# Optimization experiments

Hardware: AMD Instinct MI355X
Metric: run time of the kernel (lower is better)

Reference implementation:

```python
import jax, jax.numpy as jnp
import numpy as np

EPS = 1e-5

def _mvn(feat):
    # instance-norm style mean/std over spatial dims; torch .var is unbiased (ddof=1)
    b, c = feat.shape[:2]
    flat = feat.reshape(b, c, -1)
    mu = flat.mean(-1)[:, :, None, None]
    std = jnp.sqrt(flat.var(-1, ddof=1) + EPS)[:, :, None, None]
    return (feat - mu) / std

def setup_inputs() -> dict:
    key = jax.random.key(0)
    ks = jax.random.split(key, 10)
    B, C, H, W = 4, 512, 64, 64
    sc = 0.05
    return {
        "content": jax.random.normal(ks[0], (B, C, H, W), jnp.float32),
        "style": jax.random.normal(ks[1], (B, C, H, W), jnp.float32),
        "content_key": jax.random.normal(ks[2], (B, C, H, W), jnp.float32),
        "style_key": jax.random.normal(ks[3], (B, C, H, W), jnp.float32),
        "Wf": jax.random.normal(ks[4], (C, C), jnp.float32) * sc,
        "bf": jax.random.normal(ks[5], (C,), jnp.float32) * sc,
        "Wg": jax.random.normal(ks[6], (C, C), jnp.float32) * sc,
        "bg": jax.random.normal(ks[7], (C,), jnp.float32) * sc,
        "Wh": jax.random.normal(ks[8], (C, C), jnp.float32) * sc,
        "bh": jax.random.normal(ks[9], (C,), jnp.float32) * sc,
    }

def reference(content, style, content_key, style_key, Wf, bf, Wg, bg, Wh, bh):
    b, C, h, w = content.shape
    hs, ws = style.shape[2], style.shape[3]
    n, m = h * w, hs * ws
    # 1x1 convs are per-pixel linear maps
    Fq = jnp.einsum('oc,bcn->bno', Wf, content_key.reshape(b, -1, n)) + bf      # [b, n, ck]
    G = jnp.einsum('oc,bcn->bon', Wg, style_key.reshape(b, -1, m)) + bg[:, None]  # [b, ck, m]
    V = jnp.einsum('oc,bcn->bno', Wh, style.reshape(b, C, m)) + bh              # [b, m, C]
    S = jax.nn.softmax(jnp.einsum('bnc,bcm->bnm', Fq, G), axis=-1)              # [b, n, m]
    mean = jnp.einsum('bnm,bmc->bnc', S, V)                                     # attention-weighted mean
    m2 = jnp.einsum('bnm,bmc->bnc', S, V * V)                                   # weighted second moment
    std = jnp.sqrt(jax.nn.relu(m2 - mean * mean))
    mean = mean.reshape(b, h, w, C).transpose(0, 3, 1, 2)
    std = std.reshape(b, h, w, C).transpose(0, 3, 1, 2)
    return std * _mvn(content) + mean
```

## Files before the change

kernel.cpp:

```cpp
#include <hip/hip_runtime.h>
#include <math.h>

#define BATCH 4
#define C 512
#define N 4096
#define M 4096
#define MSPLIT 4

typedef __attribute__((ext_vector_type(8))) short short8;
typedef __attribute__((ext_vector_type(8))) __bf16 bf16x8;
typedef __attribute__((ext_vector_type(4))) float f32x4;

static __device__ __forceinline__ unsigned short f2bf(float x) {
    unsigned u = __float_as_uint(x);
    u += 0x7fff + ((u >> 16) & 1);
    return (unsigned short)(u >> 16);
}
static __device__ __forceinline__ float bf2f(unsigned short h) {
    return __uint_as_float(((unsigned)h) << 16);
}
static __device__ __forceinline__ f32x4 mfma_bf16(short8 a, short8 b, f32x4 c) {
    return __builtin_amdgcn_mfma_f32_16x16x32_bf16(
        __builtin_bit_cast(bf16x8, a), __builtin_bit_cast(bf16x8, b), c, 0, 0, 0);
}

__global__ __launch_bounds__(256) void wsplit_kernel(
    const float* __restrict__ W, unsigned short* __restrict__ hi,
    unsigned short* __restrict__ lo)
{
    int i = blockIdx.x * 256 + threadIdx.x;
    float v = W[i];
    unsigned short h = f2bf(v);
    hi[i] = h;
    lo[i] = f2bf(v - bf2f(h));
}

__global__ __launch_bounds__(256) void linear_fg_mfma(
    const float* __restrict__ in,
    const unsigned short* __restrict__ Whi, const unsigned short* __restrict__ Wlo,
    const float* __restrict__ bias,
    unsigned short* __restrict__ out_hi, unsigned short* __restrict__ out_lo)
{
    __shared__ float in_s[32][68];
    __shared__ __align__(16) unsigned short wh_s[64][40];
    __shared__ __align__(16) unsigned short wl_s[64][40];
    const int tid = threadIdx.x;
    const int n0 = blockIdx.x * 64, o0 = blockIdx.y * 64;
    const int w = tid >> 6, lane = tid & 63;
    const int wrow = w >> 1, wcol = w & 1;
    const int lr = lane & 15, q = lane >> 4;
    f32x4 acc[2][2];
    #pragma unroll
    for (int i = 0; i < 2; ++i)
        #pragma unroll
        for (int j = 0; j < 2; ++j) acc[i][j] = (f32x4){0.f, 0.f, 0.f, 0.f};

    for (int kc = 0; kc < C; kc += 32) {
        __syncthreads();
        #pragma unroll
        for (int it = 0; it < 2; ++it) {
            int idx = tid + it * 256;
            int k = idx >> 4, seg = idx & 15;
            *(float4*)&in_s[k][seg * 4] =
                *(const float4*)&in[(size_t)(kc + k) * N + n0 + seg * 4];
        }
        {
            int o = tid >> 2, sg = tid & 3;
            *(float4*)&wh_s[o][sg * 8] = *(const float4*)&Whi[(size_t)(o0 + o) * 512 + kc + sg * 8];
            *(float4*)&wl_s[o][sg * 8] = *(const float4*)&Wlo[(size_t)(o0 + o) * 512 + kc + sg * 8];
        }
        __syncthreads();
        short8 ah[2], al[2], bh[2], bl[2];
        #pragma unroll
        for (int i = 0; i < 2; ++i) {
            int n = wrow * 32 + i * 16 + lr;
            #pragma unroll
            for (int j = 0; j < 8; ++j) {
                float f = in_s[q * 8 + j][n];
                unsigned short h = f2bf(f);
                ah[i][j] = (short)h;
                al[i][j] = (short)f2bf(f - bf2f(h));
            }
        }
        #pragma unroll
        for (int j = 0; j < 2; ++j) {
            int o = wcol * 32 + j * 16 + lr;
            bh[j] = *(const short8*)&wh_s[o][q * 8];
            bl[j] = *(const short8*)&wl_s[o][q * 8];
        }
        #pragma unroll
        for (int i = 0; i < 2; ++i)
            #pragma unroll
            for (int j = 0; j < 2; ++j) {
                acc[i][j] = mfma_bf16(ah[i], bh[j], acc[i][j]);
                acc[i][j] = mfma_bf16(ah[i], bl[j], acc[i][j]);
                acc[i][j] = mfma_bf16(al[i], bh[j], acc[i][j]);
            }
    }
    #pragma unroll
    for (int i = 0; i < 2; ++i)
        #pragma unroll
        for (int j = 0; j < 2; ++j) {
            int o = o0 + wcol * 32 + j * 16 + lr;
            float bo = bias[o];
            #pragma unroll
            for (int r = 0; r < 4; ++r) {
                int n = n0 + wrow * 32 + i * 16 + q * 4 + r;
                float v = acc[i][j][r] + bo;
                unsigned short h = f2bf(v);
                out_hi[(size_t)n * 512 + o] = h;
                out_lo[(size_t)n * 512 + o] = f2bf(v - bf2f(h));
            }
        }
}

__global__ __launch_bounds__(256) void linear_v_mfma(
    const float* __restrict__ in,
    const unsigned short* __restrict__ Whi, const unsigned short* __restrict__ Wlo,
    const float* __restrict__ bias,
    unsigned short* __restrict__ vhT, unsigned short* __restrict__ v2hT,
    unsigned short* __restrict__ v2lT)
{
    __shared__ float in_s[32][68];
    __shared__ __align__(16) unsigned short wh_s[64][40];
    __shared__ __align__(16) unsigned short wl_s[64][40];
    const int tid = threadIdx.x;
    const int m0 = blockIdx.x * 64, o0 = blockIdx.y * 64;
    const int w = tid >> 6, lane = tid & 63;
    const int wrow = w >> 1, wcol = w & 1;
    const int lr = lane & 15, q = lane >> 4;
    f32x4 acc[2][2];
    #pragma unroll
    for (int i = 0; i < 2; ++i)
        #pragma unroll
        for (int j = 0; j < 2; ++j) acc[i][j] = (f32x4){0.f, 0.f, 0.f, 0.f};

    for (int kc = 0; kc < C; kc += 32) {
        __syncthreads();
        #pragma unroll
        for (int it = 0; it < 2; ++it) {
            int idx = tid + it * 256;
            int k = idx >> 4, seg = idx & 15;
            *(float4*)&in_s[k][seg * 4] =
                *(const float4*)&in[(size_t)(kc + k) * N + m0 + seg * 4];
        }
        {
            int o = tid >> 2, sg = tid & 3;
            *(float4*)&wh_s[o][sg * 8] = *(const float4*)&Whi[(size_t)(o0 + o) * 512 + kc + sg * 8];
            *(float4*)&wl_s[o][sg * 8] = *(const float4*)&Wlo[(size_t)(o0 + o) * 512 + kc + sg * 8];
        }
        __syncthreads();
        short8 ah[2], al[2], bh[2], bl[2];
        #pragma unroll
        for (int i = 0; i < 2; ++i) {
            int o = wrow * 32 + i * 16 + lr;
            ah[i] = *(const short8*)&wh_s[o][q * 8];
            al[i] = *(const short8*)&wl_s[o][q * 8];
        }
        #pragma unroll
        for (int j = 0; j < 2; ++j) {
            int m = wcol * 32 + j * 16 + lr;
            #pragma unroll
            for (int t = 0; t < 8; ++t) {
                float f = in_s[q * 8 + t][m];
                unsigned short h = f2bf(f);
                bh[j][t] = (short)h;
                bl[j][t] = (short)f2bf(f - bf2f(h));
            }
        }
        #pragma unroll
        for (int i = 0; i < 2; ++i)
            #pragma unroll
            for (int j = 0; j < 2; ++j) {
                acc[i][j] = mfma_bf16(ah[i], bh[j], acc[i][j]);
                acc[i][j] = mfma_bf16(ah[i], bl[j], acc[i][j]);
                acc[i][j] = mfma_bf16(al[i], bh[j], acc[i][j]);
            }
    }
    #pragma unroll
    for (int i = 0; i < 2; ++i)
        #pragma unroll
        for (int r = 0; r < 4; ++r) {
            int o = o0 + wrow * 32 + i * 16 + q * 4 + r;
            float bo = bias[o];
            #pragma unroll
            for (int j = 0; j < 2; ++j) {
                int m = m0 + wcol * 32 + j * 16 + lr;
                float v = acc[i][j][r] + bo;
                unsigned short vh = f2bf(v);
                float vhf = bf2f(vh);
                float vsq = vhf * vhf;
                unsigned short v2h = f2bf(vsq);
                unsigned short v2l = f2bf(vsq - bf2f(v2h));
                size_t off = (size_t)o * M + m;
                vhT[off] = vh;
                v2hT[off] = v2h;
                v2lT[off] = v2l;
            }
        }
}

__global__ __launch_bounds__(256) void logits_mfma_kernel(
    const unsigned short* __restrict__ Ah, const unsigned short* __restrict__ Al,
    const unsigned short* __restrict__ Bh, const unsigned short* __restrict__ Bl,
    float* __restrict__ S)
{
    __shared__ __align__(16) unsigned short Ah_s[128 * 40];
    __shared__ __align__(16) unsigned short Al_s[128 * 40];
    __shared__ __align__(16) unsigned short Bh_s[128 * 40];
    __shared__ __align__(16) unsigned short Bl_s[128 * 40];
    const int tid = threadIdx.x;
    const int n0 = blockIdx.y * 128, m0 = blockIdx.x * 128;
    const int w = tid >> 6, lane = tid & 63;
    const int wrow = w >> 1, wcol = w & 1;
    const int lr = lane & 15, q = lane >> 4;
    f32x4 acc[4][4];
    #pragma unroll
    for (int i = 0; i < 4; ++i)
        #pragma unroll
        for (int j = 0; j < 4; ++j)
            acc[i][j] = (f32x4){0.f, 0.f, 0.f, 0.f};

    for (int kc = 0; kc < C; kc += 32) {
        __syncthreads();
        #pragma unroll
        for (int it = 0; it < 2; ++it) {
            int idx = tid + it * 256;
            int row = idx >> 2, seg = idx & 3;
            int ldso = row * 40 + seg * 8;
            int go = kc + seg * 8;
            *(float4*)&Ah_s[ldso] = *(const float4*)&Ah[(size_t)(n0 + row) * C + go];
            *(float4*)&Al_s[ldso] = *(const float4*)&Al[(size_t)(n0 + row) * C + go];
            *(float4*)&Bh_s[ldso] = *(const float4*)&Bh[(size_t)(m0 + row) * C + go];
            *(float4*)&Bl_s[ldso] = *(const float4*)&Bl[(size_t)(m0 + row) * C + go];
        }
        __syncthreads();
        short8 ah[4], al[4], bh[4], bl[4];
        #pragma unroll
        for (int i = 0; i < 4; ++i) {
            int ro = (wrow * 64 + i * 16 + lr) * 40 + q * 8;
            int co = (wcol * 64 + i * 16 + lr) * 40 + q * 8;
            ah[i] = *(const short8*)&Ah_s[ro];
            al[i] = *(const short8*)&Al_s[ro];
            bh[i] = *(const short8*)&Bh_s[co];
            bl[i] = *(const short8*)&Bl_s[co];
        }
        #pragma unroll
        for (int i = 0; i < 4; ++i)
            #pragma unroll
            for (int j = 0; j < 4; ++j) {
                acc[i][j] = mfma_bf16(ah[i], bh[j], acc[i][j]);
                acc[i][j] = mfma_bf16(ah[i], bl[j], acc[i][j]);
                acc[i][j] = mfma_bf16(al[i], bh[j], acc[i][j]);
            }
    }
    #pragma unroll
    for (int i = 0; i < 4; ++i) {
        int nb = n0 + wrow * 64 + i * 16 + q * 4;
        #pragma unroll
        for (int j = 0; j < 4; ++j) {
            int m = m0 + wcol * 64 + j * 16 + lr;
            #pragma unroll
            for (int r = 0; r < 4; ++r)
                S[(size_t)(nb + r) * M + m] = acc[i][j][r];
        }
    }
}

__global__ __launch_bounds__(256) void rowstat_p_kernel(
    const float* __restrict__ S, unsigned short* __restrict__ P,
    float* __restrict__ rsum)
{
    const int n = blockIdx.x;
    const int tid = threadIdx.x;
    const float* row = S + (size_t)n * M;
    float v[16];
    #pragma unroll
    for (int i = 0; i < 16; ++i) v[i] = row[tid + i * 256];
    float lm = -INFINITY;
    #pragma unroll
    for (int i = 0; i < 16; ++i) lm = fmaxf(lm, v[i]);
    #pragma unroll
    for (int off = 32; off > 0; off >>= 1) lm = fmaxf(lm, __shfl_xor(lm, off, 64));
    __shared__ float red[4];
    __shared__ float redsum[4];
    const int wid = tid >> 6, lane = tid & 63;
    if (lane == 0) red[wid] = lm;
    __syncthreads();
    const float rm = fmaxf(fmaxf(red[0], red[1]), fmaxf(red[2], red[3]));
    float ls = 0.f;
    unsigned short* prow = P + (size_t)n * M;
    #pragma unroll
    for (int i = 0; i < 16; ++i) {
        float p = __expf(v[i] - rm);
        unsigned short pb = f2bf(p);
        prow[tid + i * 256] = pb;
        ls += bf2f(pb);
    }
    #pragma unroll
    for (int off = 32; off > 0; off >>= 1) ls += __shfl_xor(ls, off, 64);
    if (lane == 0) redsum[wid] = ls;
    __syncthreads();
    if (tid == 0) rsum[n] = redsum[0] + redsum[1] + redsum[2] + redsum[3];
}

__global__ __launch_bounds__(256) void apply_partial_kernel(
    const unsigned short* __restrict__ P, const unsigned short* __restrict__ VhT,
    const unsigned short* __restrict__ V2hT, const unsigned short* __restrict__ V2lT,
    float* __restrict__ accm_p, float* __restrict__ acc2_p)
{
    __shared__ __align__(16) unsigned short P_s[128 * 40];
    __shared__ __align__(16) unsigned short Vh_s[64 * 40];
    __shared__ __align__(16) unsigned short V2h_s[64 * 40];
    __shared__ __align__(16) unsigned short V2l_s[64 * 40];
    const int tid = threadIdx.x;
    const int c0 = blockIdx.x * 64, n0 = blockIdx.y * 128;
    const int z = blockIdx.z;
    const int w = tid >> 6, lane = tid & 63;
    const int wrow = w >> 1, wcol = w & 1;
    const int lr = lane & 15, q = lane >> 4;
    f32x4 accm[4][2], acc2[4][2];
    #pragma unroll
    for (int i = 0; i < 4; ++i)
        #pragma unroll
        for (int j = 0; j < 2; ++j) {
            accm[i][j] = (f32x4){0.f, 0.f, 0.f, 0.f};
            acc2[i][j] = (f32x4){0.f, 0.f, 0.f, 0.f};
        }

    const int mbeg = z * (M / MSPLIT);
    for (int mc = mbeg; mc < mbeg + M / MSPLIT; mc += 32) {
        __syncthreads();
        #pragma unroll
        for (int it = 0; it < 2; ++it) {
            int idx = tid + it * 256;
            int row = idx >> 2, seg = idx & 3;
            *(float4*)&P_s[row * 40 + seg * 8] =
                *(const float4*)&P[(size_t)(n0 + row) * M + mc + seg * 8];
        }
        {
            int row = tid >> 2, seg = tid & 3;
            int ldso = row * 40 + seg * 8;
            size_t go = (size_t)(c0 + row) * M + mc + seg * 8;
            *(float4*)&Vh_s[ldso]  = *(const float4*)&VhT[go];
            *(float4*)&V2h_s[ldso] = *(const float4*)&V2hT[go];
            *(float4*)&V2l_s[ldso] = *(const float4*)&V2lT[go];
        }
        __syncthreads();
        short8 a[4], bmat[2], b2h[2], b2l[2];
        #pragma unroll
        for (int i = 0; i < 4; ++i)
            a[i] = *(const short8*)&P_s[(wrow * 64 + i * 16 + lr) * 40 + q * 8];
        #pragma unroll
        for (int j = 0; j < 2; ++j) {
            int co = (wcol * 32 + j * 16 + lr) * 40 + q * 8;
            bmat[j] = *(const short8*)&Vh_s[co];
            b2h[j]  = *(const short8*)&V2h_s[co];
            b2l[j]  = *(const short8*)&V2l_s[co];
        }
        #pragma unroll
        for (int i = 0; i < 4; ++i)
            #pragma unroll
            for (int j = 0; j < 2; ++j) {
                accm[i][j] = mfma_bf16(a[i], bmat[j], accm[i][j]);
                acc2[i][j] = mfma_bf16(a[i], b2h[j],  acc2[i][j]);
                acc2[i][j] = mfma_bf16(a[i], b2l[j],  acc2[i][j]);
            }
    }
    const size_t pbase = (size_t)z * N * C;
    #pragma unroll
    for (int i = 0; i < 4; ++i) {
        int nb = n0 + wrow * 64 + i * 16 + q * 4;
        #pragma unroll
        for (int j = 0; j < 2; ++j) {
            int c = c0 + wcol * 32 + j * 16 + lr;
            #pragma unroll
            for (int r = 0; r < 4; ++r) {
                size_t off = pbase + (size_t)(nb + r) * C + c;
                accm_p[off] = accm[i][j][r];
                acc2_p[off] = acc2[i][j][r];
            }
        }
    }
}

__global__ __launch_bounds__(256) void combine_kernel(
    const float* __restrict__ accm_p, const float* __restrict__ acc2_p,
    const float* __restrict__ rsum, float* __restrict__ meanw,
    float* __restrict__ stdw)
{
    const size_t idx = ((size_t)blockIdx.x * 256 + threadIdx.x) * 4;
    const int n = (int)(idx >> 9);
    const float inv = 1.0f / rsum[n];
    float sm[4] = {0.f, 0.f, 0.f, 0.f}, s2[4] = {0.f, 0.f, 0.f, 0.f};
    #pragma unroll
    for (int z = 0; z < MSPLIT; ++z) {
        float4 a = *(const float4*)&accm_p[(size_t)z * N * C + idx];
        float4 b = *(const float4*)&acc2_p[(size_t)z * N * C + idx];
        sm[0] += a.x; sm[1] += a.y; sm[2] += a.z; sm[3] += a.w;
        s2[0] += b.x; s2[1] += b.y; s2[2] += b.z; s2[3] += b.w;
    }
    float4 mnv, sdv;
    float* mp = (float*)&mnv;
    float* sp = (float*)&sdv;
    #pragma unroll
    for (int k = 0; k < 4; ++k) {
        float mn = sm[k] * inv;
        float m2 = s2[k] * inv;
        mp[k] = mn;
        sp[k] = sqrtf(fmaxf(m2 - mn * mn, 0.f));
    }
    *(float4*)&meanw[idx] = mnv;
    *(float4*)&stdw[idx]  = sdv;
}

__global__ __launch_bounds__(256) void mvn_kernel(
    const float* __restrict__ content, float* __restrict__ mu, float* __restrict__ rstd)
{
    const int c = blockIdx.x;
    const int tid = threadIdx.x;
    const float* row = content + (size_t)c * N;
    float s = 0.f, ss = 0.f;
    for (int i = tid; i < N; i += 256) {
        float v = row[i];
        s += v;
        ss = fmaf(v, v, ss);
    }
    #pragma unroll
    for (int off = 32; off > 0; off >>= 1) {
        s  += __shfl_xor(s,  off, 64);
        ss += __shfl_xor(ss, off, 64);
    }
    __shared__ float rs[4], rss[4];
    const int wid = tid >> 6, lane = tid & 63;
    if (lane == 0) { rs[wid] = s; rss[wid] = ss; }
    __syncthreads();
    if (tid == 0) {
        float st = rs[0] + rs[1] + rs[2] + rs[3];
        float sst = rss[0] + rss[1] + rss[2] + rss[3];
        float m = st / (float)N;
        float var = (sst - st * st / (float)N) / (float)(N - 1);
        mu[c] = m;
        rstd[c] = rsqrtf(var + 1e-5f);
    }
}

__global__ __launch_bounds__(256) void final_kernel(
    const float* __restrict__ content, const float* __restrict__ meanw,
    const float* __restrict__ stdw, const float* __restrict__ mu,
    const float* __restrict__ rstd, float* __restrict__ out)
{
    __shared__ float mn_s[32][33], sd_s[32][33];
    const int tid = threadIdx.x;
    const int n0 = blockIdx.x * 32;
    const int c0 = blockIdx.y * 32;
    const int tx = tid & 31, ty = tid >> 5;
    #pragma unroll
    for (int i = 0; i < 4; ++i) {
        int n = ty + i * 8;
        mn_s[tx][n] = meanw[(size_t)(n0 + n) * C + c0 + tx];
        sd_s[tx][n] = stdw [(size_t)(n0 + n) * C + c0 + tx];
    }
    __syncthreads();
    #pragma unroll
    for (int i = 0; i < 4; ++i) {
        int c = ty + i * 8;
        float m = mu[c0 + c], r = rstd[c0 + c];
        size_t off = (size_t)(c0 + c) * N + n0 + tx;
        float x = content[off];
        out[off] = sd_s[c][tx] * (x - m) * r + mn_s[c][tx];
    }
}

extern "C" void kernel_launch(void* const* d_in, const int* in_sizes, int n_in,
                              void* d_out, int out_size, void* d_ws, size_t ws_size,
                              hipStream_t stream)
{
    const float* content = (const float*)d_in[0];
    const float* style   = (const float*)d_in[1];
    const float* ckey    = (const float*)d_in[2];
    const float* skey    = (const float*)d_in[3];
    const float* Wf      = (const float*)d_in[4];
    const float* bf      = (const float*)d_in[5];
    const float* Wg      = (const float*)d_in[6];
    const float* bg      = (const float*)d_in[7];
    const float* Wh      = (const float*)d_in[8];
    const float* bh      = (const float*)d_in[9];
    float* out = (float*)d_out;

    const size_t sz_w  = (size_t)512 * 512 * 2;
    const size_t sz_S  = (size_t)N * M * 4;
    const size_t sz_FG = (size_t)N * C * 2;
    const size_t sz_P  = (size_t)N * M * 2;
    const size_t sz_V  = (size_t)C * M * 2;

    char* p = (char*)d_ws;
    auto alloc = [&](size_t bytes) {
        char* r = p;
        p += (bytes + 255) & ~(size_t)255;
        return r;
    };
    unsigned short* WfH = (unsigned short*)alloc(sz_w);
    unsigned short* WfL = (unsigned short*)alloc(sz_w);
    unsigned short* WgH = (unsigned short*)alloc(sz_w);
    unsigned short* WgL = (unsigned short*)alloc(sz_w);
    unsigned short* WhH = (unsigned short*)alloc(sz_w);
    unsigned short* WhL = (unsigned short*)alloc(sz_w);
    float* S = (float*)alloc(sz_S);
    unsigned short* Fh = (unsigned short*)alloc(sz_FG);
    unsigned short* Fl = (unsigned short*)alloc(sz_FG);
    unsigned short* Gh = (unsigned short*)alloc(sz_FG);
    unsigned short* Gl = (unsigned short*)alloc(sz_FG);
    unsigned short* P    = (unsigned short*)alloc(sz_P);
    unsigned short* VhT  = (unsigned short*)alloc(sz_V);
    unsigned short* V2hT = (unsigned short*)alloc(sz_V);
    unsigned short* V2lT = (unsigned short*)alloc(sz_V);
    float* rsum  = (float*)alloc((size_t)N * 4);
    float* meanw = (float*)alloc((size_t)N * C * 4);
    float* stdw  = (float*)alloc((size_t)N * C * 4);
    float* mu    = (float*)alloc((size_t)C * 4);
    float* rstd  = (float*)alloc((size_t)C * 4);

    float* accm_p = S;
    float* acc2_p = S + (size_t)MSPLIT * N * C;

    wsplit_kernel<<<dim3(1024), 256, 0, stream>>>(Wf, WfH, WfL);
    wsplit_kernel<<<dim3(1024), 256, 0, stream>>>(Wg, WgH, WgL);
    wsplit_kernel<<<dim3(1024), 256, 0, stream>>>(Wh, WhH, WhL);

    for (int b = 0; b < BATCH; ++b) {
        const size_t fo = (size_t)b * C * N;
        linear_fg_mfma<<<dim3(N / 64, C / 64), 256, 0, stream>>>(ckey + fo, WfH, WfL, bf, Fh, Fl);
        linear_fg_mfma<<<dim3(M / 64, C / 64), 256, 0, stream>>>(skey + fo, WgH, WgL, bg, Gh, Gl);
        linear_v_mfma<<<dim3(M / 64, C / 64), 256, 0, stream>>>(style + fo, WhH, WhL, bh,
                                                                VhT, V2hT, V2lT);
        logits_mfma_kernel<<<dim3(M / 128, N / 128), 256, 0, stream>>>(Fh, Fl, Gh, Gl, S);
        rowstat_p_kernel<<<dim3(N), 256, 0, stream>>>(S, P, rsum);
        apply_partial_kernel<<<dim3(C / 64, N / 128, MSPLIT), 256, 0, stream>>>(
            P, VhT, V2hT, V2lT, accm_p, acc2_p);
        combine_kernel<<<dim3(N * C / 1024), 256, 0, stream>>>(
            accm_p, acc2_p, rsum, meanw, stdw);
        mvn_kernel<<<dim3(C), 256, 0, stream>>>(content + fo, mu, rstd);
        final_kernel<<<dim3(N / 32, C / 32), 256, 0, stream>>>(
            content + fo, meanw, stdw, mu, rstd, out + fo);
    }
}
```

Before: 1.145 ms.

## Use direct global-to-LDS loads and compute V squared splits on the fly

The logits and apply kernels now stage tiles through global_load_lds (16-byte direct-to-LDS loads) in an unpadded 32-wide LDS layout instead of loading through registers into padded rows. The V-projection kernel no longer writes the V² hi/lo bf16 arrays. The apply kernel rebuilds V² hi/lo from the bf16 V tile in registers with packed bf16 conversions, which cuts global traffic and LDS usage. The cost is extra ALU work per tile and possible LDS bank conflicts from dropping the padding.

```diff
diff --git a/kernel.cpp b/kernel.cpp
--- a/kernel.cpp
+++ b/kernel.cpp
@@ -10,6 +10,7 @@
 typedef __attribute__((ext_vector_type(8))) short short8;
 typedef __attribute__((ext_vector_type(8))) __bf16 bf16x8;
 typedef __attribute__((ext_vector_type(4))) float f32x4;
+typedef __attribute__((ext_vector_type(4))) unsigned int uint4v;
 
 static __device__ __forceinline__ unsigned short f2bf(float x) {
     unsigned u = __float_as_uint(x);
@@ -22,6 +23,16 @@
 static __device__ __forceinline__ f32x4 mfma_bf16(short8 a, short8 b, f32x4 c) {
     return __builtin_amdgcn_mfma_f32_16x16x32_bf16(
         __builtin_bit_cast(bf16x8, a), __builtin_bit_cast(bf16x8, b), c, 0, 0, 0);
+}
+static __device__ __forceinline__ void gload16(const void* g, void* l) {
+    __builtin_amdgcn_global_load_lds(
+        (const __attribute__((address_space(1))) void*)g,
+        (__attribute__((address_space(3))) void*)l, 16, 0, 0);
+}
+static __device__ __forceinline__ unsigned cvt_pk_bf16(float a, float b) {
+    unsigned r;
+    asm("v_cvt_pk_bf16_f32 %0, %1, %2" : "=v"(r) : "v"(a), "v"(b));
+    return r;
 }
 
 __global__ __launch_bounds__(256) void wsplit_kernel(
@@ -118,8 +129,7 @@
     const float* __restrict__ in,
     const unsigned short* __restrict__ Whi, const unsigned short* __restrict__ Wlo,
     const float* __restrict__ bias,
-    unsigned short* __restrict__ vhT, unsigned short* __restrict__ v2hT,
-    unsigned short* __restrict__ v2lT)
+    unsigned short* __restrict__ vhT)
 {
     __shared__ float in_s[32][68];
     __shared__ __align__(16) unsigned short wh_s[64][40];
@@ -187,15 +197,7 @@
             for (int j = 0; j < 2; ++j) {
                 int m = m0 + wcol * 32 + j * 16 + lr;
                 float v = acc[i][j][r] + bo;
-                unsigned short vh = f2bf(v);
-                float vhf = bf2f(vh);
-                float vsq = vhf * vhf;
-                unsigned short v2h = f2bf(vsq);
-                unsigned short v2l = f2bf(vsq - bf2f(v2h));
-                size_t off = (size_t)o * M + m;
-                vhT[off] = vh;
-                v2hT[off] = v2h;
-                v2lT[off] = v2l;
+                vhT[(size_t)o * M + m] = f2bf(v);
             }
         }
 }
@@ -205,15 +207,16 @@
     const unsigned short* __restrict__ Bh, const unsigned short* __restrict__ Bl,
     float* __restrict__ S)
 {
-    __shared__ __align__(16) unsigned short Ah_s[128 * 40];
-    __shared__ __align__(16) unsigned short Al_s[128 * 40];
-    __shared__ __align__(16) unsigned short Bh_s[128 * 40];
-    __shared__ __align__(16) unsigned short Bl_s[128 * 40];
+    __shared__ __align__(16) unsigned short Ah_s[128 * 32];
+    __shared__ __align__(16) unsigned short Al_s[128 * 32];
+    __shared__ __align__(16) unsigned short Bh_s[128 * 32];
+    __shared__ __align__(16) unsigned short Bl_s[128 * 32];
     const int tid = threadIdx.x;
     const int n0 = blockIdx.y * 128, m0 = blockIdx.x * 128;
     const int w = tid >> 6, lane = tid & 63;
     const int wrow = w >> 1, wcol = w & 1;
     const int lr = lane & 15, q = lane >> 4;
+    const int srow = lane >> 2, scol = (lane & 3) * 8;
     f32x4 acc[4][4];
     #pragma unroll
     for (int i = 0; i < 4; ++i)
@@ -224,22 +227,22 @@
     for (int kc = 0; kc < C; kc += 32) {
         __syncthreads();
         #pragma unroll
-        for (int it = 0; it < 2; ++it) {
-            int idx = tid + it * 256;
-            int row = idx >> 2, seg = idx & 3;
-            int ldso = row * 40 + seg * 8;
-            int go = kc + seg * 8;
-            *(float4*)&Ah_s[ldso] = *(const float4*)&Ah[(size_t)(n0 + row) * C + go];
-            *(float4*)&Al_s[ldso] = *(const float4*)&Al[(size_t)(n0 + row) * C + go];
-            *(float4*)&Bh_s[ldso] = *(const float4*)&Bh[(size_t)(m0 + row) * C + go];
-            *(float4*)&Bl_s[ldso] = *(const float4*)&Bl[(size_t)(m0 + row) * C + go];
+        for (int g2 = 0; g2 < 2; ++g2) {
+            int g = w * 2 + g2;
+            size_t ga = (size_t)(n0 + g * 16 + srow) * C + kc + scol;
+            size_t gb = (size_t)(m0 + g * 16 + srow) * C + kc + scol;
+            int lo = g * 512;
+            gload16(&Ah[ga], &Ah_s[lo]);
+            gload16(&Al[ga], &Al_s[lo]);
+            gload16(&Bh[gb], &Bh_s[lo]);
+            gload16(&Bl[gb], &Bl_s[lo]);
         }
         __syncthreads();
         short8 ah[4], al[4], bh[4], bl[4];
         #pragma unroll
         for (int i = 0; i < 4; ++i) {
-            int ro = (wrow * 64 + i * 16 + lr) * 40 + q * 8;
-            int co = (wcol * 64 + i * 16 + lr) * 40 + q * 8;
+            int ro = (wrow * 64 + i * 16 + lr) * 32 + q * 8;
+            int co = (wcol * 64 + i * 16 + lr) * 32 + q * 8;
             ah[i] = *(const short8*)&Ah_s[ro];
             al[i] = *(const short8*)&Al_s[ro];
             bh[i] = *(const short8*)&Bh_s[co];
@@ -306,19 +309,17 @@
 
 __global__ __launch_bounds__(256) void apply_partial_kernel(
     const unsigned short* __restrict__ P, const unsigned short* __restrict__ VhT,
-    const unsigned short* __restrict__ V2hT, const unsigned short* __restrict__ V2lT,
     float* __restrict__ accm_p, float* __restrict__ acc2_p)
 {
-    __shared__ __align__(16) unsigned short P_s[128 * 40];
-    __shared__ __align__(16) unsigned short Vh_s[64 * 40];
-    __shared__ __align__(16) unsigned short V2h_s[64 * 40];
-    __shared__ __align__(16) unsigned short V2l_s[64 * 40];
+    __shared__ __align__(16) unsigned short P_s[128 * 32];
+    __shared__ __align__(16) unsigned short Vh_s[64 * 32];
     const int tid = threadIdx.x;
     const int c0 = blockIdx.x * 64, n0 = blockIdx.y * 128;
     const int z = blockIdx.z;
     const int w = tid >> 6, lane = tid & 63;
     const int wrow = w >> 1, wcol = w & 1;
     const int lr = lane & 15, q = lane >> 4;
+    const int srow = lane >> 2, scol = (lane & 3) * 8;
     f32x4 accm[4][2], acc2[4][2];
     #pragma unroll
     for (int i = 0; i < 4; ++i)
@@ -332,39 +333,42 @@
     for (int mc = mbeg; mc < mbeg + M / MSPLIT; mc += 32) {
         __syncthreads();
         #pragma unroll
-        for (int it = 0; it < 2; ++it) {
-            int idx = tid + it * 256;
-            int row = idx >> 2, seg = idx & 3;
-            *(float4*)&P_s[row * 40 + seg * 8] =
-                *(const float4*)&P[(size_t)(n0 + row) * M + mc + seg * 8];
-        }
-        {
-            int row = tid >> 2, seg = tid & 3;
-            int ldso = row * 40 + seg * 8;
-            size_t go = (size_t)(c0 + row) * M + mc + seg * 8;
-            *(float4*)&Vh_s[ldso]  = *(const float4*)&VhT[go];
-            *(float4*)&V2h_s[ldso] = *(const float4*)&V2hT[go];
-            *(float4*)&V2l_s[ldso] = *(const float4*)&V2lT[go];
-        }
-        __syncthreads();
-        short8 a[4], bmat[2], b2h[2], b2l[2];
+        for (int g2 = 0; g2 < 2; ++g2) {
+            int g = w * 2 + g2;
+            gload16(&P[(size_t)(n0 + g * 16 + srow) * M + mc + scol], &P_s[g * 512]);
+        }
+        gload16(&VhT[(size_t)(c0 + w * 16 + srow) * M + mc + scol], &Vh_s[w * 512]);
+        __syncthreads();
+        short8 a[4], bh[2], b2h[2], b2l[2];
         #pragma unroll
         for (int i = 0; i < 4; ++i)
-            a[i] = *(const short8*)&P_s[(wrow * 64 + i * 16 + lr) * 40 + q * 8];
+            a[i] = *(const short8*)&P_s[(wrow * 64 + i * 16 + lr) * 32 + q * 8];
         #pragma unroll
         for (int j = 0; j < 2; ++j) {
-            int co = (wcol * 32 + j * 16 + lr) * 40 + q * 8;
-            bmat[j] = *(const short8*)&Vh_s[co];
-            b2h[j]  = *(const short8*)&V2h_s[co];
-            b2l[j]  = *(const short8*)&V2l_s[co];
+            bh[j] = *(const short8*)&Vh_s[(wcol * 32 + j * 16 + lr) * 32 + q * 8];
+            uint4v u = __builtin_bit_cast(uint4v, bh[j]);
+            uint4v hv, lv;
+            #pragma unroll
+            for (int t = 0; t < 4; ++t) {
+                float v0 = __uint_as_float(u[t] << 16);
+                float v1 = __uint_as_float(u[t] & 0xffff0000u);
+                float s0 = v0 * v0, s1 = v1 * v1;
+                unsigned hh = cvt_pk_bf16(s0, s1);
+                float r0 = s0 - __uint_as_float(hh << 16);
+                float r1 = s1 - __uint_as_float(hh & 0xffff0000u);
+                hv[t] = hh;
+                lv[t] = cvt_pk_bf16(r0, r1);
+            }
+            b2h[j] = __builtin_bit_cast(short8, hv);
+            b2l[j] = __builtin_bit_cast(short8, lv);
         }
         #pragma unroll
         for (int i = 0; i < 4; ++i)
             #pragma unroll
             for (int j = 0; j < 2; ++j) {
-                accm[i][j] = mfma_bf16(a[i], bmat[j], accm[i][j]);
-                acc2[i][j] = mfma_bf16(a[i], b2h[j],  acc2[i][j]);
-                acc2[i][j] = mfma_bf16(a[i], b2l[j],  acc2[i][j]);
+                accm[i][j] = mfma_bf16(a[i], bh[j],  accm[i][j]);
+                acc2[i][j] = mfma_bf16(a[i], b2h[j], acc2[i][j]);
+                acc2[i][j] = mfma_bf16(a[i], b2l[j], acc2[i][j]);
             }
     }
     const size_t pbase = (size_t)z * N * C;
@@ -513,8 +517,6 @@
     unsigned short* Gl = (unsigned short*)alloc(sz_FG);
     unsigned short* P    = (unsigned short*)alloc(sz_P);
     unsigned short* VhT  = (unsigned short*)alloc(sz_V);
-    unsigned short* V2hT = (unsigned short*)alloc(sz_V);
-    unsigned short* V2lT = (unsigned short*)alloc(sz_V);
     float* rsum  = (float*)alloc((size_t)N * 4);
     float* meanw = (float*)alloc((size_t)N * C * 4);
     float* stdw  = (float*)alloc((size_t)N * C * 4);
@@ -532,12 +534,11 @@
         const size_t fo = (size_t)b * C * N;
         linear_fg_mfma<<<dim3(N / 64, C / 64), 256, 0, stream>>>(ckey + fo, WfH, WfL, bf, Fh, Fl);
         linear_fg_mfma<<<dim3(M / 64, C / 64), 256, 0, stream>>>(skey + fo, WgH, WgL, bg, Gh, Gl);
-        linear_v_mfma<<<dim3(M / 64, C / 64), 256, 0, stream>>>(style + fo, WhH, WhL, bh,
-                                                                VhT, V2hT, V2lT);
+        linear_v_mfma<<<dim3(M / 64, C / 64), 256, 0, stream>>>(style + fo, WhH, WhL, bh, VhT);
         logits_mfma_kernel<<<dim3(M / 128, N / 128), 256, 0, stream>>>(Fh, Fl, Gh, Gl, S);
         rowstat_p_kernel<<<dim3(N), 256, 0, stream>>>(S, P, rsum);
         apply_partial_kernel<<<dim3(C / 64, N / 128, MSPLIT), 256, 0, stream>>>(
-            P, VhT, V2hT, V2lT, accm_p, acc2_p);
+            P, VhT, accm_p, acc2_p);
         combine_kernel<<<dim3(N * C / 1024), 256, 0, stream>>>(
             accm_p, acc2_p, rsum, meanw, stdw);
         mvn_kernel<<<dim3(C), 256, 0, stream>>>(content + fo, mu, rstd);
```

Result: faster. 1.091 ms (-4.7%).
